# Performance work log

Hardware: AMD Instinct MI355X
Metric: run time of the kernel (lower is better)

Reference implementation:

```python
import jax, jax.numpy as jnp
import numpy as np

MODEL_DIM = 1024
NUM_HEADS = 16
HEAD_DIM = MODEL_DIM // NUM_HEADS
BATCH = 16
KEY_LEN = 4096


def setup_inputs() -> dict:
    key = jax.random.key(0)
    ks = jax.random.split(key, 10)
    u = lambda k, shape: jax.random.uniform(k, shape, jnp.float32, -0.5, 0.5)
    return {
        "hidden_states": jax.random.normal(ks[0], (BATCH, 1, MODEL_DIM), jnp.float32),
        "key_value_states": jax.random.normal(ks[1], (BATCH, KEY_LEN, MODEL_DIM), jnp.float32),
        "Wq": u(ks[2], (MODEL_DIM, MODEL_DIM)), "bq": u(ks[3], (MODEL_DIM,)),
        "Wk": u(ks[4], (MODEL_DIM, MODEL_DIM)), "bk": u(ks[5], (MODEL_DIM,)),
        "Wv": u(ks[6], (MODEL_DIM, MODEL_DIM)), "bv": u(ks[7], (MODEL_DIM,)),
        "Wo": u(ks[8], (MODEL_DIM, MODEL_DIM)), "bo": u(ks[9], (MODEL_DIM,)),
    }


def reference(hidden_states, key_value_states, Wq, bq, Wk, bk, Wv, bv, Wo, bo):
    B, K = key_value_states.shape[0], key_value_states.shape[1]
    H, Dh = NUM_HEADS, HEAD_DIM
    # projections (nn.Linear: x @ W.T + b)
    q = hidden_states @ Wq.T + bq            # [B, 1, H*Dh]
    k = key_value_states @ Wk.T + bk         # [B, K, H*Dh]
    v = key_value_states @ Wv.T + bv         # [B, K, H*Dh]
    # split heads
    q = q.reshape(B, 1, H, Dh).transpose(0, 2, 1, 3)   # [B, H, 1, Dh]
    k = k.reshape(B, K, H, Dh).transpose(0, 2, 1, 3)   # [B, H, K, Dh]
    v = v.reshape(B, K, H, Dh).transpose(0, 2, 1, 3)   # [B, H, K, Dh]
    q = q / jnp.sqrt(jnp.asarray(Dh, q.dtype))
    # scores: [B, H, K] (query_len == 1, squeezed)
    scores = jnp.einsum("bhqd,bhkd->bhqk", q, k)[:, :, 0, :]
    # Hardtanh(min_val=0, max_val=1) gate instead of softmax; dropout p=0
    attn = jnp.clip(scores, 0.0, 1.0)                  # [B, H, K]
    # broadcast-multiply with value, merge heads back
    context = attn[..., None] * v                      # [B, H, K, Dh]
    context = context.transpose(0, 2, 1, 3).reshape(B, K, H * Dh)
    output = context @ Wo.T + bo                       # [B, K, model_dim]
    return output
```

## Files before the change

### kernel.cpp

```cpp
#include <hip/hip_runtime.h>
#include <hip/hip_bf16.h>
#include <stdint.h>

typedef __bf16 bf16x8 __attribute__((ext_vector_type(8)));
typedef __bf16 bf16x4 __attribute__((ext_vector_type(4)));
typedef float  f32x4  __attribute__((ext_vector_type(4)));

#define B_  16
#define KL  4096
#define D_  1024
#define NH  16
#define NROWS (B_*KL)

__device__ __forceinline__ void gload_lds16(const void* g, void* l) {
  __builtin_amdgcn_global_load_lds(
      (__attribute__((address_space(1))) void*)g,
      (__attribute__((address_space(3))) void*)l, 16, 0, 0);
}


__global__ __launch_bounds__(256) void conv_w_kernel(const float* __restrict__ wv,
                                                     const float* __restrict__ wo,
                                                     __bf16* __restrict__ dv,
                                                     __bf16* __restrict__ do_) {
  const bool second = blockIdx.x >= 1024;
  const int i = (second ? blockIdx.x - 1024 : blockIdx.x) * 256 + threadIdx.x;
  const float* s = second ? wo : wv;
  __bf16* d = second ? do_ : dv;
  float4 v = reinterpret_cast<const float4*>(s)[i];
  bf16x4 o;
  o[0] = (__bf16)v.x; o[1] = (__bf16)v.y; o[2] = (__bf16)v.z; o[3] = (__bf16)v.w;
  *reinterpret_cast<bf16x4*>(d + (size_t)i * 4) = o;
}

__global__ __launch_bounds__(256) void qproj_kernel(const float* __restrict__ hs,
                                                    const float* __restrict__ Wq,
                                                    const float* __restrict__ bq,
                                                    float* __restrict__ q) {
  int gid = blockIdx.x * 256 + threadIdx.x;
  int b = gid >> 10, j = gid & 1023;
  const float* x = hs + (size_t)b * D_;
  const float* w = Wq + (size_t)j * D_;
  float acc = 0.f;
  for (int i = 0; i < D_; i += 4) {
    float4 xv = *reinterpret_cast<const float4*>(x + i);
    float4 wv = *reinterpret_cast<const float4*>(w + i);
    acc += xv.x*wv.x + xv.y*wv.y + xv.z*wv.z + xv.w*wv.w;
  }
  q[gid] = (acc + bq[j]) * 0.125f;
}

__global__ __launch_bounds__(256) void wqeff_kernel(const float* __restrict__ q,
                                                    const float* __restrict__ Wk,
                                                    const float* __restrict__ bk,
                                                    __bf16* __restrict__ whi,
                                                    __bf16* __restrict__ wlo,
                                                    float* __restrict__ cb) {
  const int h = blockIdx.x, b = blockIdx.y;
  const int tid = threadIdx.x;
  __shared__ float ql[64];
  if (tid < 64) ql[tid] = q[(size_t)b * D_ + h * 64 + tid];
  __syncthreads();
  float a0 = 0, a1 = 0, a2 = 0, a3 = 0;
  for (int d = 0; d < 64; ++d) {
    float qv = ql[d];
    const float* wr = Wk + (size_t)(h * 64 + d) * D_;
    a0 += qv * wr[tid];
    a1 += qv * wr[tid + 256];
    a2 += qv * wr[tid + 512];
    a3 += qv * wr[tid + 768];
  }
  const size_t base = ((size_t)b * NH + h) * D_;
  float a[4] = {a0, a1, a2, a3};
#pragma unroll
  for (int j = 0; j < 4; ++j) {
    __bf16 hi = (__bf16)a[j];
    whi[base + j * 256 + tid] = hi;
    wlo[base + j * 256 + tid] = (__bf16)(a[j] - (float)hi);
  }
  if (tid < 64) {
    float p = ql[tid] * bk[h * 64 + tid];
    p += __shfl_down(p, 32); p += __shfl_down(p, 16); p += __shfl_down(p, 8);
    p += __shfl_down(p, 4);  p += __shfl_down(p, 2);  p += __shfl_down(p, 1);
    if (tid == 0) cb[b * NH + h] = p;
  }
}

__global__ __launch_bounds__(256) void scores_mfma_kernel(
    const float* __restrict__ kvs,
    const __bf16* __restrict__ whi,
    const __bf16* __restrict__ wlo,
    const float* __restrict__ cb,
    float* __restrict__ attn,
    __bf16* __restrict__ kvd) {
  const int b = blockIdx.y;
  const int tid = threadIdx.x;
  const int lane = tid & 63, wv = tid >> 6;
  const int r16 = lane & 15, kgrp = lane >> 4;
  const int row0 = blockIdx.x * 64 + wv * 16;
  const size_t grow = (size_t)b * KL + row0;

  const float* xrow = kvs + (grow + r16) * D_ + kgrp * 8;
  __bf16*      krow = kvd + (grow + r16) * D_ + kgrp * 8;
  const __bf16* wh = whi + ((size_t)b * NH + r16) * D_ + kgrp * 8;
  const __bf16* wl = wlo + ((size_t)b * NH + r16) * D_ + kgrp * 8;

  f32x4 acc0 = {}, acc1 = {};

#define SPROC(xx0, xx1, kk)                                                     \
  {                                                                             \
    bf16x8 bh = *reinterpret_cast<const bf16x8*>(wh + (kk));                    \
    bf16x8 bl = *reinterpret_cast<const bf16x8*>(wl + (kk));                    \
    float xs[8] = {xx0.x, xx0.y, xx0.z, xx0.w, xx1.x, xx1.y, xx1.z, xx1.w};     \
    bf16x8 hi, lo;                                                              \
    _Pragma("unroll") for (int i = 0; i < 8; ++i) {                             \
      __bf16 h = (__bf16)xs[i];                                                 \
      hi[i] = h;                                                                \
      lo[i] = (__bf16)(xs[i] - (float)h);                                       \
    }                                                                           \
    *reinterpret_cast<bf16x8*>(krow + (kk)) = hi;                               \
    acc0 = __builtin_amdgcn_mfma_f32_16x16x32_bf16(hi, bh, acc0, 0, 0, 0);      \
    acc1 = __builtin_amdgcn_mfma_f32_16x16x32_bf16(hi, bl, acc1, 0, 0, 0);      \
    acc1 = __builtin_amdgcn_mfma_f32_16x16x32_bf16(lo, bh, acc1, 0, 0, 0);      \
  }

  float4 xa0 = *reinterpret_cast<const float4*>(xrow);
  float4 xa1 = *reinterpret_cast<const float4*>(xrow + 4);
  float4 xb0 = *reinterpret_cast<const float4*>(xrow + 32);
  float4 xb1 = *reinterpret_cast<const float4*>(xrow + 36);
  for (int k0 = 0; k0 < D_; k0 += 64) {
    float4 na0, na1, nb0, nb1;
    if (k0 + 64 < D_) {
      na0 = *reinterpret_cast<const float4*>(xrow + k0 + 64);
      na1 = *reinterpret_cast<const float4*>(xrow + k0 + 68);
      nb0 = *reinterpret_cast<const float4*>(xrow + k0 + 96);
      nb1 = *reinterpret_cast<const float4*>(xrow + k0 + 100);
    }
    SPROC(xa0, xa1, k0);
    SPROC(xb0, xb1, k0 + 32);
    xa0 = na0; xa1 = na1; xb0 = nb0; xb1 = nb1;
  }
#undef SPROC
  const float c = cb[b * NH + r16];
#pragma unroll
  for (int r = 0; r < 4; ++r) {
    const int orow = row0 + kgrp * 4 + r;
    float s = acc0[r] + acc1[r] + c;
    attn[((size_t)b * KL + orow) * NH + r16] = fminf(fmaxf(s, 0.f), 1.f);
  }
}

template <bool GATE>
__global__ __launch_bounds__(512, 2) void gemm_nt(const __bf16* __restrict__ A,
                                                  const __bf16* __restrict__ Bt,
                                                  const float* __restrict__ bias,
                                                  const float* __restrict__ gate,
                                                  void* __restrict__ Cp) {
  __shared__ __bf16 As[2][256 * 64];
  __shared__ __bf16 Bs[2][256 * 64];
  const int tid = threadIdx.x;
  const int lane = tid & 63, wid = tid >> 6;
  const int wm = wid >> 2, wn = wid & 3;
  const int r16 = lane & 15, kgrp = lane >> 4;
  const int bswz = (blockIdx.x & 7) * 128 + (blockIdx.x >> 3);
  const int m0 = (bswz >> 2) * 256;
  const int n0 = (bswz & 3) * 256;

  const int srow = lane >> 3;
  const int scol = ((lane & 7) ^ srow) * 8;

  const int sw0 = ((kgrp) ^ (r16 & 7)) * 8;
  const int sw1 = ((4 + kgrp) ^ (r16 & 7)) * 8;

  f32x4 acc[8][4] = {};

#define STAGE_HALF(dstbuf, srcp, base0, h, k0)                                  \
  {                                                                             \
    _Pragma("unroll") for (int j = 0; j < 2; ++j) {                             \
      const int c = (h) * 16 + wid * 2 + j;                                     \
      gload_lds16((srcp) + (size_t)((base0) + c * 8 + srow) * D_ + (k0) + scol, \
                  &(dstbuf)[c * 512]);                                          \
    }                                                                           \
  }

#define LOAD_BV(Bb, sw)                                                         \
  _Pragma("unroll") for (int nh = 0; nh < 2; ++nh)                              \
    _Pragma("unroll") for (int g = 0; g < 2; ++g)                               \
      bv[nh * 2 + g] = *reinterpret_cast<const bf16x8*>(                        \
          &(Bb)[(nh * 128 + wn * 32 + g * 16 + r16) * 64 + (sw)]);

#define LOAD_AV(Ab, mh, sw)                                                     \
  _Pragma("unroll") for (int f = 0; f < 4; ++f)                                 \
    av[f] = *reinterpret_cast<const bf16x8*>(                                   \
        &(Ab)[((mh) * 128 + wm * 64 + f * 16 + r16) * 64 + (sw)]);

#define MFMA_PHASE(mh)                                                          \
  {                                                                             \
    __builtin_amdgcn_s_setprio(1);                                              \
    _Pragma("unroll") for (int f = 0; f < 4; ++f)                               \
      _Pragma("unroll") for (int q = 0; q < 4; ++q)                             \
        acc[(mh) * 4 + f][q] = __builtin_amdgcn_mfma_f32_16x16x32_bf16(         \
            av[f], bv[q], acc[(mh) * 4 + f][q], 0, 0, 0);                       \
    __builtin_amdgcn_s_setprio(0);                                              \
  }

#define WAITLGKM()                                                              \
  asm volatile("s_waitcnt lgkmcnt(0)" ::: "memory");                            \
  __builtin_amdgcn_sched_barrier(0);

  STAGE_HALF(Bs[0], Bt, n0, 0, 0);
  STAGE_HALF(Bs[0], Bt, n0, 1, 0);
  STAGE_HALF(As[0], A,  m0, 0, 0);
  STAGE_HALF(As[0], A,  m0, 1, 0);
  asm volatile("s_waitcnt vmcnt(2)" ::: "memory");
  __builtin_amdgcn_s_barrier();

  const int NT = D_ / 64;
  for (int t = 0; t < NT; ++t) {
    __bf16* Ab = (t & 1) ? As[1] : As[0];
    __bf16* Bb = (t & 1) ? Bs[1] : Bs[0];
    __bf16* An = (t & 1) ? As[0] : As[1];
    __bf16* Bn = (t & 1) ? Bs[0] : Bs[1];
    const int k1 = (t + 1) * 64;
    const bool pf = (t < NT - 1);
    bf16x8 bv[4], av[4];

    LOAD_BV(Bb, sw0);
    LOAD_AV(Ab, 0, sw0);
    if (pf) STAGE_HALF(Bn, Bt, n0, 0, k1);
    __builtin_amdgcn_s_barrier();
    WAITLGKM();
    MFMA_PHASE(0);
    if (pf) asm volatile("s_waitcnt vmcnt(2)" ::: "memory");
    else    asm volatile("s_waitcnt vmcnt(0)" ::: "memory");
    __builtin_amdgcn_s_barrier();
    LOAD_AV(Ab, 1, sw0);
    if (pf) STAGE_HALF(Bn, Bt, n0, 1, k1);
    __builtin_amdgcn_s_barrier();
    WAITLGKM();
    MFMA_PHASE(1);
    __builtin_amdgcn_s_barrier();
    LOAD_BV(Bb, sw1);
    LOAD_AV(Ab, 0, sw1);
    if (pf) STAGE_HALF(An, A, m0, 0, k1);
    __builtin_amdgcn_s_barrier();
    WAITLGKM();
    MFMA_PHASE(0);
    __builtin_amdgcn_s_barrier();
    LOAD_AV(Ab, 1, sw1);
    if (pf) STAGE_HALF(An, A, m0, 1, k1);
    __builtin_amdgcn_s_barrier();
    WAITLGKM();
    MFMA_PHASE(1);
    if (pf) asm volatile("s_waitcnt vmcnt(2)" ::: "memory");
    __builtin_amdgcn_s_barrier();
  }

#pragma unroll
  for (int mh = 0; mh < 2; ++mh) {
#pragma unroll
    for (int f = 0; f < 4; ++f) {
      const int row0 = m0 + mh * 128 + wm * 64 + f * 16 + kgrp * 4;
#pragma unroll
      for (int nh = 0; nh < 2; ++nh) {
#pragma unroll
        for (int g = 0; g < 2; ++g) {
          const int col = n0 + nh * 128 + wn * 32 + g * 16 + r16;
          const float bc = bias[col];
          const int head = col >> 6;
          f32x4 v = acc[mh * 4 + f][nh * 2 + g];
#pragma unroll
          for (int r = 0; r < 4; ++r) {
            const int row = row0 + r;
            if constexpr (GATE) {
              float gg = gate[(size_t)row * NH + head];
              ((__bf16*)Cp)[(size_t)row * D_ + col] = (__bf16)((v[r] + bc) * gg);
            } else {
              ((float*)Cp)[(size_t)row * D_ + col] = v[r] + bc;
            }
          }
        }
      }
    }
  }
#undef STAGE_HALF
#undef LOAD_BV
#undef LOAD_AV
#undef MFMA_PHASE
#undef WAITLGKM
}

extern "C" void kernel_launch(void* const* d_in, const int* in_sizes, int n_in,
                              void* d_out, int out_size, void* d_ws, size_t ws_size,
                              hipStream_t stream) {
  const float* hs  = (const float*)d_in[0];
  const float* kvs = (const float*)d_in[1];
  const float* Wq  = (const float*)d_in[2];
  const float* bq  = (const float*)d_in[3];
  const float* Wk  = (const float*)d_in[4];
  const float* bk  = (const float*)d_in[5];
  const float* Wv  = (const float*)d_in[6];
  const float* bv  = (const float*)d_in[7];
  const float* Wo  = (const float*)d_in[8];
  const float* bo  = (const float*)d_in[9];
  float* out = (float*)d_out;

  char* w = (char*)d_ws;
  __bf16* ctx  = (__bf16*)w;  w += (size_t)NROWS * D_ * 2;
  float*  attn = (float*)w;   w += (size_t)NROWS * NH * 4;
  __bf16* WvB  = (__bf16*)w;  w += (size_t)D_ * D_ * 2;
  __bf16* WoB  = (__bf16*)w;  w += (size_t)D_ * D_ * 2;
  __bf16* whi  = (__bf16*)w;  w += (size_t)B_ * NH * D_ * 2;
  __bf16* wlo  = (__bf16*)w;  w += (size_t)B_ * NH * D_ * 2;
  float*  qbuf = (float*)w;   w += (size_t)B_ * D_ * 4;
  float*  cbuf = (float*)w;   w += B_ * NH * 4;

  __bf16* kvsB = (__bf16*)d_out;

  conv_w_kernel<<<2048, 256, 0, stream>>>(Wv, Wo, WvB, WoB);
  qproj_kernel<<<64, 256, 0, stream>>>(hs, Wq, bq, qbuf);
  wqeff_kernel<<<dim3(NH, B_), 256, 0, stream>>>(qbuf, Wk, bk, whi, wlo, cbuf);
  scores_mfma_kernel<<<dim3(KL / 64, B_), 256, 0, stream>>>(kvs, whi, wlo, cbuf, attn, kvsB);
  gemm_nt<true ><<<1024, 512, 0, stream>>>(kvsB, WvB, bv, attn, ctx);
  gemm_nt<false><<<1024, 512, 0, stream>>>(ctx, WoB, bo, (const float*)nullptr, (void*)out);
}
```

Measured before the change: 476.5 us.

## Fuse q projection into wqeff and split scores K-dimension across two wave groups

The separate q-projection kernel is removed and folded into wqeff, where each block computes its own 64 q values from hidden states staged in shared memory, eliminating a launch and the q buffer. The scores kernel now uses 512 threads, with two groups of waves each covering half of the 1024-wide reduction and combining partial MFMA results through shared memory. This gives twice as many waves to hide the latency of streaming the fp32 key/value input. The cost is a block barrier plus a shared-memory reduction in scores, and redundant Wq reads in wqeff, since each batch block recomputes its head's q slice.

```diff
diff --git a/kernel.cpp b/kernel.cpp
--- a/kernel.cpp
+++ b/kernel.cpp
@@ -33,24 +33,9 @@
   *reinterpret_cast<bf16x4*>(d + (size_t)i * 4) = o;
 }
 
-__global__ __launch_bounds__(256) void qproj_kernel(const float* __restrict__ hs,
+__global__ __launch_bounds__(256) void wqeff_kernel(const float* __restrict__ hs,
                                                     const float* __restrict__ Wq,
                                                     const float* __restrict__ bq,
-                                                    float* __restrict__ q) {
-  int gid = blockIdx.x * 256 + threadIdx.x;
-  int b = gid >> 10, j = gid & 1023;
-  const float* x = hs + (size_t)b * D_;
-  const float* w = Wq + (size_t)j * D_;
-  float acc = 0.f;
-  for (int i = 0; i < D_; i += 4) {
-    float4 xv = *reinterpret_cast<const float4*>(x + i);
-    float4 wv = *reinterpret_cast<const float4*>(w + i);
-    acc += xv.x*wv.x + xv.y*wv.y + xv.z*wv.z + xv.w*wv.w;
-  }
-  q[gid] = (acc + bq[j]) * 0.125f;
-}
-
-__global__ __launch_bounds__(256) void wqeff_kernel(const float* __restrict__ q,
                                                     const float* __restrict__ Wk,
                                                     const float* __restrict__ bk,
                                                     __bf16* __restrict__ whi,
@@ -58,8 +43,27 @@
                                                     float* __restrict__ cb) {
   const int h = blockIdx.x, b = blockIdx.y;
   const int tid = threadIdx.x;
+  __shared__ float hsl[D_];
   __shared__ float ql[64];
-  if (tid < 64) ql[tid] = q[(size_t)b * D_ + h * 64 + tid];
+  {
+    float4 v = reinterpret_cast<const float4*>(hs + (size_t)b * D_)[tid];
+    hsl[tid * 4] = v.x; hsl[tid * 4 + 1] = v.y;
+    hsl[tid * 4 + 2] = v.z; hsl[tid * 4 + 3] = v.w;
+  }
+  __syncthreads();
+  {
+    const int d = tid >> 2, seg = tid & 3;
+    const float* wr = Wq + (size_t)(h * 64 + d) * D_ + seg * 256;
+    const float* xs = hsl + seg * 256;
+    float p = 0.f;
+    for (int i = 0; i < 256; i += 4) {
+      float4 wv4 = *reinterpret_cast<const float4*>(wr + i);
+      p += xs[i] * wv4.x + xs[i + 1] * wv4.y + xs[i + 2] * wv4.z + xs[i + 3] * wv4.w;
+    }
+    p += __shfl_xor(p, 1);
+    p += __shfl_xor(p, 2);
+    if (seg == 0) ql[d] = (p + bq[h * 64 + d]) * 0.125f;
+  }
   __syncthreads();
   float a0 = 0, a1 = 0, a2 = 0, a3 = 0;
   for (int d = 0; d < 64; ++d) {
@@ -86,24 +90,28 @@
   }
 }
 
-__global__ __launch_bounds__(256) void scores_mfma_kernel(
+__global__ __launch_bounds__(512) void scores_mfma_kernel(
     const float* __restrict__ kvs,
     const __bf16* __restrict__ whi,
     const __bf16* __restrict__ wlo,
     const float* __restrict__ cb,
     float* __restrict__ attn,
     __bf16* __restrict__ kvd) {
+  __shared__ f32x4 part[4][64];
   const int b = blockIdx.y;
   const int tid = threadIdx.x;
   const int lane = tid & 63, wv = tid >> 6;
+  const int rg = wv & 3;
+  const int kh = wv >> 2;
   const int r16 = lane & 15, kgrp = lane >> 4;
-  const int row0 = blockIdx.x * 64 + wv * 16;
+  const int row0 = blockIdx.x * 64 + rg * 16;
   const size_t grow = (size_t)b * KL + row0;
-
-  const float* xrow = kvs + (grow + r16) * D_ + kgrp * 8;
-  __bf16*      krow = kvd + (grow + r16) * D_ + kgrp * 8;
-  const __bf16* wh = whi + ((size_t)b * NH + r16) * D_ + kgrp * 8;
-  const __bf16* wl = wlo + ((size_t)b * NH + r16) * D_ + kgrp * 8;
+  const int kbase = kh * 512;
+
+  const float* xrow = kvs + (grow + r16) * D_ + kbase + kgrp * 8;
+  __bf16*      krow = kvd + (grow + r16) * D_ + kbase + kgrp * 8;
+  const __bf16* wh = whi + ((size_t)b * NH + r16) * D_ + kbase + kgrp * 8;
+  const __bf16* wl = wlo + ((size_t)b * NH + r16) * D_ + kbase + kgrp * 8;
 
   f32x4 acc0 = {}, acc1 = {};
 
@@ -128,9 +136,9 @@
   float4 xa1 = *reinterpret_cast<const float4*>(xrow + 4);
   float4 xb0 = *reinterpret_cast<const float4*>(xrow + 32);
   float4 xb1 = *reinterpret_cast<const float4*>(xrow + 36);
-  for (int k0 = 0; k0 < D_; k0 += 64) {
+  for (int k0 = 0; k0 < 512; k0 += 64) {
     float4 na0, na1, nb0, nb1;
-    if (k0 + 64 < D_) {
+    if (k0 + 64 < 512) {
       na0 = *reinterpret_cast<const float4*>(xrow + k0 + 64);
       na1 = *reinterpret_cast<const float4*>(xrow + k0 + 68);
       nb0 = *reinterpret_cast<const float4*>(xrow + k0 + 96);
@@ -141,12 +149,23 @@
     xa0 = na0; xa1 = na1; xb0 = nb0; xb1 = nb1;
   }
 #undef SPROC
-  const float c = cb[b * NH + r16];
-#pragma unroll
-  for (int r = 0; r < 4; ++r) {
-    const int orow = row0 + kgrp * 4 + r;
-    float s = acc0[r] + acc1[r] + c;
-    attn[((size_t)b * KL + orow) * NH + r16] = fminf(fmaxf(s, 0.f), 1.f);
+
+  if (kh == 1) {
+    f32x4 s = acc0;
+#pragma unroll
+    for (int r = 0; r < 4; ++r) s[r] += acc1[r];
+    part[rg][lane] = s;
+  }
+  __syncthreads();
+  if (kh == 0) {
+    f32x4 p = part[rg][lane];
+    const float c = cb[b * NH + r16];
+#pragma unroll
+    for (int r = 0; r < 4; ++r) {
+      const int orow = row0 + kgrp * 4 + r;
+      float s = acc0[r] + acc1[r] + p[r] + c;
+      attn[((size_t)b * KL + orow) * NH + r16] = fminf(fmaxf(s, 0.f), 1.f);
+    }
   }
 }
 
@@ -312,15 +331,13 @@
   __bf16* WoB  = (__bf16*)w;  w += (size_t)D_ * D_ * 2;
   __bf16* whi  = (__bf16*)w;  w += (size_t)B_ * NH * D_ * 2;
   __bf16* wlo  = (__bf16*)w;  w += (size_t)B_ * NH * D_ * 2;
-  float*  qbuf = (float*)w;   w += (size_t)B_ * D_ * 4;
   float*  cbuf = (float*)w;   w += B_ * NH * 4;
 
   __bf16* kvsB = (__bf16*)d_out;
 
   conv_w_kernel<<<2048, 256, 0, stream>>>(Wv, Wo, WvB, WoB);
-  qproj_kernel<<<64, 256, 0, stream>>>(hs, Wq, bq, qbuf);
-  wqeff_kernel<<<dim3(NH, B_), 256, 0, stream>>>(qbuf, Wk, bk, whi, wlo, cbuf);
-  scores_mfma_kernel<<<dim3(KL / 64, B_), 256, 0, stream>>>(kvs, whi, wlo, cbuf, attn, kvsB);
+  wqeff_kernel<<<dim3(NH, B_), 256, 0, stream>>>(hs, Wq, bq, Wk, bk, whi, wlo, cbuf);
+  scores_mfma_kernel<<<dim3(KL / 64, B_), 512, 0, stream>>>(kvs, whi, wlo, cbuf, attn, kvsB);
   gemm_nt<true ><<<1024, 512, 0, stream>>>(kvsB, WvB, bv, attn, ctx);
   gemm_nt<false><<<1024, 512, 0, stream>>>(ctx, WoB, bo, (const float*)nullptr, (void*)out);
 }
```

New measurement: 443.5 us. -6.9%, faster.
